# Kernel tuning notes

Measured on AMD Instinct MI355X. Metric: run time of the kernel, lower is better.

## Reference

```python
import jax, jax.numpy as jnp
import numpy as np

DIM = 768
N_HEADS = 12
HEAD_DIM = DIM // N_HEADS

def setup_inputs() -> dict:
    key = jax.random.key(0)
    ks = jax.random.split(key, 5)
    B, N = 8, 1024
    s = 0.02
    x = jax.random.normal(ks[0], (B, N, DIM), dtype=jnp.float32)
    W_qkv = jax.random.normal(ks[1], (DIM, 3 * DIM), dtype=jnp.float32) * s
    b_qkv = jnp.zeros((3 * DIM,), dtype=jnp.float32)
    W_proj = jax.random.normal(ks[2], (DIM, DIM), dtype=jnp.float32) * s
    b_proj = jnp.zeros((DIM,), dtype=jnp.float32)
    return {"x": x, "W_qkv": W_qkv, "b_qkv": b_qkv, "W_proj": W_proj, "b_proj": b_proj}

def reference(x, W_qkv, b_qkv, W_proj, b_proj):
    B, N, D = x.shape
    qkv = x @ W_qkv + b_qkv                                   # [B,N,3D]
    qkv = qkv.reshape(B, N, 3, N_HEADS, HEAD_DIM)
    q, k, v = qkv[:, :, 0], qkv[:, :, 1], qkv[:, :, 2]        # [B,N,H,hd]
    q = q.transpose(0, 2, 1, 3)                               # [B,H,N,hd]
    k = k.transpose(0, 2, 1, 3)
    v = v.transpose(0, 2, 1, 3)
    scores = jnp.einsum('bhqd,bhkd->bhqk', q, k) / jnp.sqrt(jnp.float32(HEAD_DIM))
    attn = jax.nn.softmax(scores, axis=-1)
    out = jnp.einsum('bhqk,bhkd->bhqd', attn, v)              # [B,H,N,hd]
    out = out.transpose(0, 2, 1, 3).reshape(B, N, D)
    return out @ W_proj + b_proj
```

## Files before the change

### kernel.cpp

```cpp
#include <hip/hip_runtime.h>
#include <hip/hip_bf16.h>


typedef __bf16 bf16x8 __attribute__((ext_vector_type(8)));
typedef float f32x4 __attribute__((ext_vector_type(4)));

#define MFMA16(a, b, c) __builtin_amdgcn_mfma_f32_16x16x32_bf16(a, b, c, 0, 0, 0)

#if defined(__has_builtin) && __has_builtin(__builtin_amdgcn_exp2f)
#define EXP2(x) __builtin_amdgcn_exp2f(x)
#else
#define EXP2(x) exp2f(x)
#endif

__device__ inline __bf16 to_bf16(float f) {
  __hip_bfloat16 h = __float2bfloat16(f);
  return *reinterpret_cast<__bf16*>(&h);
}

__device__ __forceinline__ void gload16(const void* g, void* l) {
  __builtin_amdgcn_global_load_lds(
      (const __attribute__((address_space(1))) unsigned int*)(unsigned long long)g,
      (__attribute__((address_space(3))) unsigned int*)(unsigned long long)l,
      16, 0, 0);
}

__global__ void ws_diag_kernel(float* out, int n, float val) {
  int i = blockIdx.x * 256 + threadIdx.x;
  if (i < n) out[i] = val;
}

__global__ __launch_bounds__(256) void prep_kernel(
    const float* __restrict__ x, __hip_bfloat16* __restrict__ xc,
    const float* __restrict__ Wqkv, __hip_bfloat16* __restrict__ WqkvT,
    const float* __restrict__ Wproj, __hip_bfloat16* __restrict__ WprojT) {
  __shared__ __hip_bfloat16 tile[32][33];
  const int b = blockIdx.x;
  if (b < 3072) {
    int i = b * 256 + threadIdx.x;
    float4 a = ((const float4*)x)[i * 2], c = ((const float4*)x)[i * 2 + 1];
    __hip_bfloat16 o[8] = {__float2bfloat16(a.x), __float2bfloat16(a.y),
                           __float2bfloat16(a.z), __float2bfloat16(a.w),
                           __float2bfloat16(c.x), __float2bfloat16(c.y),
                           __float2bfloat16(c.z), __float2bfloat16(c.w)};
    *(int4*)(xc + (size_t)i * 8) = *(const int4*)o;
    return;
  }
  const float* W;
  __hip_bfloat16* Wt;
  int rows, cols, bx, by;
  if (b < 4800) {
    int idx = b - 3072;
    W = Wqkv; Wt = WqkvT; rows = 768; cols = 2304;
    bx = idx % 72; by = idx / 72;
  } else {
    int idx = b - 4800;
    W = Wproj; Wt = WprojT; rows = 768; cols = 768;
    bx = idx % 24; by = idx / 24;
  }
  const int tc = bx * 32, tr = by * 32;
  const int tx = threadIdx.x & 31, ty = threadIdx.x >> 5;
#pragma unroll
  for (int i = 0; i < 4; ++i) {
    int r = ty + i * 8;
    tile[r][tx] = __float2bfloat16(W[(size_t)(tr + r) * cols + tc + tx]);
  }
  __syncthreads();
#pragma unroll
  for (int i = 0; i < 4; ++i) {
    int r = ty + i * 8;
    Wt[(size_t)(tc + r) * rows + tr + tx] = tile[tx][r];
  }
}

__global__ __launch_bounds__(256) void vtrans_kernel(
    const __hip_bfloat16* __restrict__ Vrow, __hip_bfloat16* __restrict__ Vt) {
  constexpr int LP = 72;
  __shared__ __bf16 tile[64 * LP];
  const int tid = threadIdx.x;
  const int bh = blockIdx.x;
  const int n0 = blockIdx.y * 64;
  const size_t base = (size_t)bh << 16;
#pragma unroll
  for (int i = 0; i < 2; ++i) {
    int s = tid + 256 * i;
    int r = s >> 3, c8 = (s & 7) * 8;
    *(int4*)(&tile[r * LP + c8]) =
        *(const int4*)(Vrow + base + (size_t)(n0 + r) * 64 + c8);
  }
  __syncthreads();
#pragma unroll
  for (int i = 0; i < 2; ++i) {
    int s = tid + 256 * i;
    int d = s >> 3, n8 = (s & 7) * 8;
    __bf16 o[8];
#pragma unroll
    for (int j = 0; j < 8; ++j) o[j] = tile[(n8 + j) * LP + d];
    *(int4*)(Vt + base + ((size_t)d << 10) + n0 + n8) = *(const int4*)o;
  }
}

constexpr int GK = 768;

__global__ __launch_bounds__(256) void gemm_qkv_kernel(
    const __hip_bfloat16* __restrict__ A,
    const __hip_bfloat16* __restrict__ Bt,
    const float* __restrict__ bias,
    __hip_bfloat16* __restrict__ Qw,
    __hip_bfloat16* __restrict__ Kw,
    __hip_bfloat16* __restrict__ Vw) {
  __shared__ __align__(16) __bf16 As[128 * 32];
  __shared__ __align__(16) __bf16 Bs[128 * 32];
  const int tid = threadIdx.x;
  const int lane = tid & 63, wave = tid >> 6;
  const int wr = wave >> 1, wc = wave & 1;
  const int m0 = blockIdx.x * 128, n0 = blockIdx.y * 128;
  const int fr = lane & 15, q4 = lane >> 4;

  const int r4 = lane >> 2, c8 = (lane & 3) * 8;
  const __hip_bfloat16* ga0 = A + (size_t)(m0 + wave * 32 + r4) * GK + c8;
  const __hip_bfloat16* gb0 = Bt + (size_t)(n0 + wave * 32 + r4) * GK + c8;
  __bf16* la0 = &As[wave * 1024];
  __bf16* lb0 = &Bs[wave * 1024];

  f32x4 acc[4][4] = {};

  for (int kt = 0; kt < GK / 32; ++kt) {
    __syncthreads();
    gload16(ga0 + kt * 32, la0);
    gload16(ga0 + kt * 32 + 16 * GK, la0 + 512);
    gload16(gb0 + kt * 32, lb0);
    gload16(gb0 + kt * 32 + 16 * GK, lb0 + 512);
    __syncthreads();
    bf16x8 af[4], bfr[4];
#pragma unroll
    for (int i = 0; i < 4; ++i)
      af[i] = *(const bf16x8*)(&As[(wr * 64 + i * 16 + fr) * 32 + q4 * 8]);
#pragma unroll
    for (int j = 0; j < 4; ++j)
      bfr[j] = *(const bf16x8*)(&Bs[(wc * 64 + j * 16 + fr) * 32 + q4 * 8]);
#pragma unroll
    for (int i = 0; i < 4; ++i)
#pragma unroll
      for (int j = 0; j < 4; ++j)
        acc[i][j] = MFMA16(af[i], bfr[j], acc[i][j]);
  }

#pragma unroll
  for (int j = 0; j < 4; ++j) {
    int col = n0 + wc * 64 + j * 16 + fr;
    int which = col / 768;
    int rem = col - which * 768;
    int h = rem >> 6, d = rem & 63;
    float bv = bias[col];
    __hip_bfloat16* dst = (which == 0) ? Qw : (which == 1) ? Kw : Vw;
    float scale = (which == 0) ? 0.18033688011112042f : 1.0f;
#pragma unroll
    for (int i = 0; i < 4; ++i) {
#pragma unroll
      for (int r = 0; r < 4; ++r) {
        int row = m0 + wr * 64 + i * 16 + q4 * 4 + r;
        int bb = row >> 10, nn = row & 1023;
        float v = (acc[i][j][r] + bv) * scale;
        dst[(((size_t)(bb * 12 + h) * 1024 + nn) << 6) + d] = __float2bfloat16(v);
      }
    }
  }
}

__global__ __launch_bounds__(256) void gemm_proj_kernel(
    const __hip_bfloat16* __restrict__ A,
    const __hip_bfloat16* __restrict__ Bt,
    const float* __restrict__ bias,
    float* __restrict__ out) {
  __shared__ __align__(16) __bf16 As[128 * 32];
  __shared__ __align__(16) __bf16 Bs[128 * 32];
  const int tid = threadIdx.x;
  const int lane = tid & 63, wave = tid >> 6;
  const int wr = wave >> 1, wc = wave & 1;
  const int m0 = blockIdx.x * 128, n0 = blockIdx.y * 128;
  const int fr = lane & 15, q4 = lane >> 4;

  const int r4 = lane >> 2, c8 = (lane & 3) * 8;
  const __hip_bfloat16* ga0 = A + (size_t)(m0 + wave * 32 + r4) * GK + c8;
  const __hip_bfloat16* gb0 = Bt + (size_t)(n0 + wave * 32 + r4) * GK + c8;
  __bf16* la0 = &As[wave * 1024];
  __bf16* lb0 = &Bs[wave * 1024];

  f32x4 acc[4][4] = {};

  for (int kt = 0; kt < GK / 32; ++kt) {
    __syncthreads();
    gload16(ga0 + kt * 32, la0);
    gload16(ga0 + kt * 32 + 16 * GK, la0 + 512);
    gload16(gb0 + kt * 32, lb0);
    gload16(gb0 + kt * 32 + 16 * GK, lb0 + 512);
    __syncthreads();
    bf16x8 af[4], bfr[4];
#pragma unroll
    for (int i = 0; i < 4; ++i)
      af[i] = *(const bf16x8*)(&As[(wr * 64 + i * 16 + fr) * 32 + q4 * 8]);
#pragma unroll
    for (int j = 0; j < 4; ++j)
      bfr[j] = *(const bf16x8*)(&Bs[(wc * 64 + j * 16 + fr) * 32 + q4 * 8]);
#pragma unroll
    for (int i = 0; i < 4; ++i)
#pragma unroll
      for (int j = 0; j < 4; ++j)
        acc[i][j] = MFMA16(af[i], bfr[j], acc[i][j]);
  }

#pragma unroll
  for (int j = 0; j < 4; ++j) {
    int col = n0 + wc * 64 + j * 16 + fr;
    float bv = bias[col];
#pragma unroll
    for (int i = 0; i < 4; ++i) {
#pragma unroll
      for (int r = 0; r < 4; ++r) {
        int row = m0 + wr * 64 + i * 16 + q4 * 4 + r;
        out[(size_t)row * 768 + col] = acc[i][j][r] + bv;
      }
    }
  }
}

__global__ __launch_bounds__(512) void attn_kernel(
    const __hip_bfloat16* __restrict__ Qw,
    const __hip_bfloat16* __restrict__ Kw,
    const __hip_bfloat16* __restrict__ Vt,
    __hip_bfloat16* __restrict__ O) {
  constexpr int LP = 72;
  __shared__ __bf16 smem[18432];
  __bf16* Qs = smem;
  __bf16* K1 = smem;
  __bf16* V1 = smem + 4608;
  __bf16* K0 = smem + 9216;
  __bf16* V0 = smem + 13824;
  const int tid = threadIdx.x;
  const int lane = tid & 63, wave = tid >> 6;
  const int fr = lane & 15, q4 = lane >> 4;
  const int bh = blockIdx.x % 96, qt = blockIdx.x / 96;
  const __hip_bfloat16* Qb = Qw + ((size_t)bh * 1024 + qt * 128) * 64;
  const __hip_bfloat16* Kb = Kw + (size_t)bh * 65536;
  const __hip_bfloat16* Vb = Vt + (size_t)bh * 65536;

  const int krow = tid >> 3, kc = (tid & 7) * 8;
  int4 kregA = *(const int4*)(Kb + (size_t)krow * 64 + kc);
  int4 vregA = *(const int4*)(Vb + ((size_t)krow << 10) + kc);

#pragma unroll
  for (int i = 0; i < 2; ++i) {
    int s = tid + 512 * i;
    int row = s >> 3, c = (s & 7) * 8;
    *(int4*)(&Qs[row * LP + c]) = *(const int4*)(Qb + row * 64 + c);
  }
  __syncthreads();
  bf16x8 qf[2];
#pragma unroll
  for (int ks = 0; ks < 2; ++ks)
    qf[ks] = *(const bf16x8*)(&Qs[(wave * 16 + fr) * LP + ks * 32 + q4 * 8]);

  float l_i = 0.f;
  f32x4 accO[4] = {};

  const int sc8 = tid & 7;
  const int sbase = ((sc8 >> 2) << 5) | ((sc8 & 1) << 4) | (((sc8 >> 1) & 1) << 2);

  *(int4*)(&K0[krow * LP + kc]) = kregA;
  *(int2*)(&V0[krow * LP + sbase]) = make_int2(vregA.x, vregA.y);
  *(int2*)(&V0[krow * LP + sbase + 8]) = make_int2(vregA.z, vregA.w);
  int4 kregB = *(const int4*)(Kb + (size_t)(64 + krow) * 64 + kc);
  int4 vregB = *(const int4*)(Vb + ((size_t)krow << 10) + 64 + kc);
  __syncthreads();

  auto compute_tile = [&](const __bf16* Kbuf, const __bf16* Vbuf) {
    f32x4 scT[4];
    __builtin_amdgcn_s_setprio(1);
#pragma unroll
    for (int nt = 0; nt < 4; ++nt) {
      bf16x8 kf0 = *(const bf16x8*)(&Kbuf[(nt * 16 + fr) * LP + q4 * 8]);
      bf16x8 kf1 = *(const bf16x8*)(&Kbuf[(nt * 16 + fr) * LP + 32 + q4 * 8]);
      f32x4 z = {};
      z = MFMA16(kf0, qf[0], z);
      scT[nt] = MFMA16(kf1, qf[1], z);
    }
    __builtin_amdgcn_s_setprio(0);
    float rs = 0.f;
#pragma unroll
    for (int nt = 0; nt < 4; ++nt)
#pragma unroll
      for (int r = 0; r < 4; ++r) {
        float p = EXP2(scT[nt][r]);
        scT[nt][r] = p;
        rs += p;
      }
    l_i += rs;
#pragma unroll
    for (int ks = 0; ks < 2; ++ks) {
      bf16x8 pf;
#pragma unroll
      for (int e = 0; e < 4; ++e) {
        pf[e] = to_bf16(scT[2 * ks][e]);
        pf[4 + e] = to_bf16(scT[2 * ks + 1][e]);
      }
      __builtin_amdgcn_s_setprio(1);
#pragma unroll
      for (int dt = 0; dt < 4; ++dt) {
        bf16x8 vf = *(const bf16x8*)(&Vbuf[(dt * 16 + fr) * LP + ks * 32 + q4 * 8]);
        accO[dt] = MFMA16(pf, vf, accO[dt]);
      }
      __builtin_amdgcn_s_setprio(0);
    }
  };

  for (int kt2 = 0; kt2 < 16; kt2 += 2) {
    compute_tile(K0, V0);
    *(int4*)(&K1[krow * LP + kc]) = kregB;
    *(int2*)(&V1[krow * LP + sbase]) = make_int2(vregB.x, vregB.y);
    *(int2*)(&V1[krow * LP + sbase + 8]) = make_int2(vregB.z, vregB.w);
    if (kt2 + 2 < 16) {
      kregA = *(const int4*)(Kb + (size_t)((kt2 + 2) * 64 + krow) * 64 + kc);
      vregA = *(const int4*)(Vb + ((size_t)krow << 10) + (kt2 + 2) * 64 + kc);
    }
    __syncthreads();
    compute_tile(K1, V1);
    if (kt2 + 2 < 16) {
      *(int4*)(&K0[krow * LP + kc]) = kregA;
      *(int2*)(&V0[krow * LP + sbase]) = make_int2(vregA.x, vregA.y);
      *(int2*)(&V0[krow * LP + sbase + 8]) = make_int2(vregA.z, vregA.w);
      kregB = *(const int4*)(Kb + (size_t)((kt2 + 3) * 64 + krow) * 64 + kc);
      vregB = *(const int4*)(Vb + ((size_t)krow << 10) + (kt2 + 3) * 64 + kc);
      __syncthreads();
    }
  }

  l_i += __shfl_xor(l_i, 16, 64);
  l_i += __shfl_xor(l_i, 32, 64);
  float lrow[4];
#pragma unroll
  for (int r = 0; r < 4; ++r) lrow[r] = __shfl(l_i, q4 * 4 + r, 64);

  const int h = bh % 12, bb = bh / 12;
#pragma unroll
  for (int dt = 0; dt < 4; ++dt)
#pragma unroll
    for (int r = 0; r < 4; ++r) {
      int row = bb * 1024 + qt * 128 + wave * 16 + q4 * 4 + r;
      int col = h * 64 + dt * 16 + fr;
      O[(size_t)row * 768 + col] = __float2bfloat16(accO[dt][r] / lrow[r]);
    }
}

extern "C" void kernel_launch(void* const* d_in, const int* in_sizes, int n_in,
                              void* d_out, int out_size, void* d_ws, size_t ws_size,
                              hipStream_t stream) {
  const float* x     = (const float*)d_in[0];
  const float* Wqkv  = (const float*)d_in[1];
  const float* bqkv  = (const float*)d_in[2];
  const float* Wproj = (const float*)d_in[3];
  const float* bproj = (const float*)d_in[4];
  float* out = (float*)d_out;

  constexpr size_t NEEDED = 55050240;
  if (ws_size < NEEDED) {
    ws_diag_kernel<<<(out_size + 255) / 256, 256, 0, stream>>>(
        out, out_size, (float)(ws_size >> 20));
    return;
  }

  char* ws = (char*)d_ws;
  __hip_bfloat16* WqkvT  = (__hip_bfloat16*)(ws);
  __hip_bfloat16* WprojT = (__hip_bfloat16*)(ws + 3538944);
  __hip_bfloat16* Qw     = (__hip_bfloat16*)(ws + 4718592);
  __hip_bfloat16* Kw     = (__hip_bfloat16*)(ws + 17301504);
  __hip_bfloat16* Vrow   = (__hip_bfloat16*)(ws + 29884416);
  __hip_bfloat16* xc     = (__hip_bfloat16*)(ws + 42467328);
  __hip_bfloat16* Vt     = xc;
  __hip_bfloat16* attnO  = Vrow;

  prep_kernel<<<5376, 256, 0, stream>>>(x, xc, Wqkv, WqkvT, Wproj, WprojT);
  gemm_qkv_kernel<<<dim3(64, 18), 256, 0, stream>>>(xc, WqkvT, bqkv, Qw, Kw, Vrow);
  vtrans_kernel<<<dim3(96, 16), 256, 0, stream>>>(Vrow, Vt);
  attn_kernel<<<dim3(96 * 8), 512, 0, stream>>>(Qw, Kw, Vt, attnO);
  gemm_proj_kernel<<<dim3(64, 6), 256, 0, stream>>>(attnO, WprojT, bproj, out);
}
```

Before: 191.0 us.

## Fuse V transpose into QKV GEMM epilogue with pre-swizzled tile layout

The separate V transpose kernel is removed. The QKV GEMM epilogue now writes V directly in a per-64-key-tile transposed, pre-swizzled layout, so the attention kernel loads V with plain 16-byte copies into LDS. This saves one kernel launch and a full read and write pass over V. The cost is a more complex epilogue with 8-byte scattered stores, and the attention output buffer now aliases xc.

```diff
diff --git a/kernel.cpp b/kernel.cpp
--- a/kernel.cpp
+++ b/kernel.cpp
@@ -73,33 +73,6 @@
   }
 }
 
-__global__ __launch_bounds__(256) void vtrans_kernel(
-    const __hip_bfloat16* __restrict__ Vrow, __hip_bfloat16* __restrict__ Vt) {
-  constexpr int LP = 72;
-  __shared__ __bf16 tile[64 * LP];
-  const int tid = threadIdx.x;
-  const int bh = blockIdx.x;
-  const int n0 = blockIdx.y * 64;
-  const size_t base = (size_t)bh << 16;
-#pragma unroll
-  for (int i = 0; i < 2; ++i) {
-    int s = tid + 256 * i;
-    int r = s >> 3, c8 = (s & 7) * 8;
-    *(int4*)(&tile[r * LP + c8]) =
-        *(const int4*)(Vrow + base + (size_t)(n0 + r) * 64 + c8);
-  }
-  __syncthreads();
-#pragma unroll
-  for (int i = 0; i < 2; ++i) {
-    int s = tid + 256 * i;
-    int d = s >> 3, n8 = (s & 7) * 8;
-    __bf16 o[8];
-#pragma unroll
-    for (int j = 0; j < 8; ++j) o[j] = tile[(n8 + j) * LP + d];
-    *(int4*)(Vt + base + ((size_t)d << 10) + n0 + n8) = *(const int4*)o;
-  }
-}
-
 constexpr int GK = 768;
 
 __global__ __launch_bounds__(256) void gemm_qkv_kernel(
@@ -108,7 +81,7 @@
     const float* __restrict__ bias,
     __hip_bfloat16* __restrict__ Qw,
     __hip_bfloat16* __restrict__ Kw,
-    __hip_bfloat16* __restrict__ Vw) {
+    __hip_bfloat16* __restrict__ Vs) {
   __shared__ __align__(16) __bf16 As[128 * 32];
   __shared__ __align__(16) __bf16 Bs[128 * 32];
   const int tid = threadIdx.x;
@@ -146,23 +119,47 @@
         acc[i][j] = MFMA16(af[i], bfr[j], acc[i][j]);
   }
 
-#pragma unroll
-  for (int j = 0; j < 4; ++j) {
-    int col = n0 + wc * 64 + j * 16 + fr;
-    int which = col / 768;
-    int rem = col - which * 768;
-    int h = rem >> 6, d = rem & 63;
-    float bv = bias[col];
-    __hip_bfloat16* dst = (which == 0) ? Qw : (which == 1) ? Kw : Vw;
-    float scale = (which == 0) ? 0.18033688011112042f : 1.0f;
-#pragma unroll
-    for (int i = 0; i < 4; ++i) {
-#pragma unroll
-      for (int r = 0; r < 4; ++r) {
-        int row = m0 + wr * 64 + i * 16 + q4 * 4 + r;
-        int bb = row >> 10, nn = row & 1023;
-        float v = (acc[i][j][r] + bv) * scale;
-        dst[(((size_t)(bb * 12 + h) * 1024 + nn) << 6) + d] = __float2bfloat16(v);
+  if (n0 < 1536) {
+#pragma unroll
+    for (int j = 0; j < 4; ++j) {
+      int col = n0 + wc * 64 + j * 16 + fr;
+      int which = (col >= 768) ? 1 : 0;
+      int rem = col - which * 768;
+      int h = rem >> 6, d = rem & 63;
+      float bv = bias[col];
+      __hip_bfloat16* dst = (which == 0) ? Qw : Kw;
+      float scale = (which == 0) ? 0.18033688011112042f : 1.0f;
+#pragma unroll
+      for (int i = 0; i < 4; ++i) {
+#pragma unroll
+        for (int r = 0; r < 4; ++r) {
+          int row = m0 + wr * 64 + i * 16 + q4 * 4 + r;
+          int bb = row >> 10, nn = row & 1023;
+          float v = (acc[i][j][r] + bv) * scale;
+          dst[(((size_t)(bb * 12 + h) * 1024 + nn) << 6) + d] = __float2bfloat16(v);
+        }
+      }
+    }
+  } else {
+    const int rowbase = m0 + wr * 64;
+    const int bb = rowbase >> 10;
+    const int ktile = (rowbase & 1023) >> 6;
+    const int hq = (q4 & 1) * 8;
+#pragma unroll
+    for (int j = 0; j < 4; ++j) {
+      int rem = (n0 - 1536) + wc * 64 + j * 16 + fr;
+      int h = rem >> 6, d = rem & 63;
+      float bv = bias[n0 + wc * 64 + j * 16 + fr];
+      __hip_bfloat16* vb =
+          Vs + (((size_t)(bb * 12 + h)) << 16) + ktile * 4096 + d * 64;
+#pragma unroll
+      for (int i = 0; i < 4; ++i) {
+        int c = i * 2 + (q4 >> 1);
+        int pos = (((c >> 2) << 5) | ((c & 1) << 4) | (((c >> 1) & 1) << 2)) + hq;
+        __hip_bfloat16 o[4];
+#pragma unroll
+        for (int r = 0; r < 4; ++r) o[r] = __float2bfloat16(acc[i][j][r] + bv);
+        *(int2*)(vb + pos) = *(const int2*)o;
       }
     }
   }
@@ -228,7 +225,7 @@
 __global__ __launch_bounds__(512) void attn_kernel(
     const __hip_bfloat16* __restrict__ Qw,
     const __hip_bfloat16* __restrict__ Kw,
-    const __hip_bfloat16* __restrict__ Vt,
+    const __hip_bfloat16* __restrict__ Vs,
     __hip_bfloat16* __restrict__ O) {
   constexpr int LP = 72;
   __shared__ __bf16 smem[18432];
@@ -243,11 +240,11 @@
   const int bh = blockIdx.x % 96, qt = blockIdx.x / 96;
   const __hip_bfloat16* Qb = Qw + ((size_t)bh * 1024 + qt * 128) * 64;
   const __hip_bfloat16* Kb = Kw + (size_t)bh * 65536;
-  const __hip_bfloat16* Vb = Vt + (size_t)bh * 65536;
+  const __hip_bfloat16* Vb = Vs + (size_t)bh * 65536;
 
   const int krow = tid >> 3, kc = (tid & 7) * 8;
   int4 kregA = *(const int4*)(Kb + (size_t)krow * 64 + kc);
-  int4 vregA = *(const int4*)(Vb + ((size_t)krow << 10) + kc);
+  int4 vregA = *(const int4*)(Vb + (size_t)krow * 64 + kc);
 
 #pragma unroll
   for (int i = 0; i < 2; ++i) {
@@ -264,14 +261,10 @@
   float l_i = 0.f;
   f32x4 accO[4] = {};
 
-  const int sc8 = tid & 7;
-  const int sbase = ((sc8 >> 2) << 5) | ((sc8 & 1) << 4) | (((sc8 >> 1) & 1) << 2);
-
   *(int4*)(&K0[krow * LP + kc]) = kregA;
-  *(int2*)(&V0[krow * LP + sbase]) = make_int2(vregA.x, vregA.y);
-  *(int2*)(&V0[krow * LP + sbase + 8]) = make_int2(vregA.z, vregA.w);
+  *(int4*)(&V0[krow * LP + kc]) = vregA;
   int4 kregB = *(const int4*)(Kb + (size_t)(64 + krow) * 64 + kc);
-  int4 vregB = *(const int4*)(Vb + ((size_t)krow << 10) + 64 + kc);
+  int4 vregB = *(const int4*)(Vb + 4096 + (size_t)krow * 64 + kc);
   __syncthreads();
 
   auto compute_tile = [&](const __bf16* Kbuf, const __bf16* Vbuf) {
@@ -317,20 +310,18 @@
   for (int kt2 = 0; kt2 < 16; kt2 += 2) {
     compute_tile(K0, V0);
     *(int4*)(&K1[krow * LP + kc]) = kregB;
-    *(int2*)(&V1[krow * LP + sbase]) = make_int2(vregB.x, vregB.y);
-    *(int2*)(&V1[krow * LP + sbase + 8]) = make_int2(vregB.z, vregB.w);
+    *(int4*)(&V1[krow * LP + kc]) = vregB;
     if (kt2 + 2 < 16) {
       kregA = *(const int4*)(Kb + (size_t)((kt2 + 2) * 64 + krow) * 64 + kc);
-      vregA = *(const int4*)(Vb + ((size_t)krow << 10) + (kt2 + 2) * 64 + kc);
+      vregA = *(const int4*)(Vb + (size_t)(kt2 + 2) * 4096 + (size_t)krow * 64 + kc);
     }
     __syncthreads();
     compute_tile(K1, V1);
     if (kt2 + 2 < 16) {
       *(int4*)(&K0[krow * LP + kc]) = kregA;
-      *(int2*)(&V0[krow * LP + sbase]) = make_int2(vregA.x, vregA.y);
-      *(int2*)(&V0[krow * LP + sbase + 8]) = make_int2(vregA.z, vregA.w);
+      *(int4*)(&V0[krow * LP + kc]) = vregA;
       kregB = *(const int4*)(Kb + (size_t)((kt2 + 3) * 64 + krow) * 64 + kc);
-      vregB = *(const int4*)(Vb + ((size_t)krow << 10) + (kt2 + 3) * 64 + kc);
+      vregB = *(const int4*)(Vb + (size_t)(kt2 + 3) * 4096 + (size_t)krow * 64 + kc);
       __syncthreads();
     }
   }
@@ -374,14 +365,12 @@
   __hip_bfloat16* WprojT = (__hip_bfloat16*)(ws + 3538944);
   __hip_bfloat16* Qw     = (__hip_bfloat16*)(ws + 4718592);
   __hip_bfloat16* Kw     = (__hip_bfloat16*)(ws + 17301504);
-  __hip_bfloat16* Vrow   = (__hip_bfloat16*)(ws + 29884416);
+  __hip_bfloat16* Vs     = (__hip_bfloat16*)(ws + 29884416);
   __hip_bfloat16* xc     = (__hip_bfloat16*)(ws + 42467328);
-  __hip_bfloat16* Vt     = xc;
-  __hip_bfloat16* attnO  = Vrow;
+  __hip_bfloat16* attnO  = xc;
 
   prep_kernel<<<5376, 256, 0, stream>>>(x, xc, Wqkv, WqkvT, Wproj, WprojT);
-  gemm_qkv_kernel<<<dim3(64, 18), 256, 0, stream>>>(xc, WqkvT, bqkv, Qw, Kw, Vrow);
-  vtrans_kernel<<<dim3(96, 16), 256, 0, stream>>>(Vrow, Vt);
-  attn_kernel<<<dim3(96 * 8), 512, 0, stream>>>(Qw, Kw, Vt, attnO);
+  gemm_qkv_kernel<<<dim3(64, 18), 256, 0, stream>>>(xc, WqkvT, bqkv, Qw, Kw, Vs);
+  attn_kernel<<<dim3(96 * 8), 512, 0, stream>>>(Qw, Kw, Vs, attnO);
   gemm_proj_kernel<<<dim3(64, 6), 256, 0, stream>>>(attnO, WprojT, bproj, out);
 }
```

After: 196.0 us. +2.6%, slower.
